# Performance work log

Hardware: AMD Instinct MI355X
Metric: run time of the kernel (lower is better)

## Reference

```python
import jax, jax.numpy as jnp
import numpy as np

T, B, M, A, H = 2048, 128, 32, 32, 64
G = M + A + H  # gate input features (mass_in_gates=True)


def _l1norm(a):
    # F.normalize(p=1, dim=-1): a / max(sum|a|, 1e-12); a is sigmoid output (>0)
    return a / jnp.maximum(jnp.sum(jnp.abs(a), axis=-1, keepdims=True), 1e-12)


def setup_inputs() -> dict:
    key = jax.random.key(0)
    ks = jax.random.split(key, 5)
    ortho = jax.nn.initializers.orthogonal()
    return {
        "x_m": jax.random.uniform(ks[0], (T, B, M), dtype=jnp.float32),
        "x_a": jax.random.normal(ks[1], (T, B, A), dtype=jnp.float32),
        "Wi": ortho(ks[2], (G, M * H), jnp.float32),  # input gate
        "bi": jnp.zeros((M * H,), jnp.float32),
        "Wr": ortho(ks[3], (G, H * H), jnp.float32),  # redistribution
        "br": jnp.zeros((H * H,), jnp.float32),
        "Wo": ortho(ks[4], (G, H), jnp.float32),      # output gate
        "bo": jnp.zeros((H,), jnp.float32),
    }


def reference(x_m, x_a, Wi, bi, Wr, br, Wo, bo):
    def step(c, xs):
        xt_m, xt_a = xs  # [B,M], [B,A]
        # NOTE: torch c.norm(1) (no dim) = scalar L1 norm of whole [B,H] tensor
        cn = c / (jnp.sum(jnp.abs(c)) + 1e-5)
        feat = jnp.concatenate([xt_m, xt_a, cn], axis=-1)  # [B,G]
        i = _l1norm(jax.nn.sigmoid(feat @ Wi + bi).reshape(-1, M, H))  # [B,M,H]
        r = _l1norm(jax.nn.sigmoid(feat @ Wr + br).reshape(-1, H, H))  # [B,H,H]
        o = jax.nn.sigmoid(feat @ Wo + bo)                              # [B,H]
        m_new = jnp.einsum('bm,bmh->bh', xt_m, i) + jnp.einsum('bk,bkh->bh', c, r)
        m_out = o * m_new
        c_new = (1.0 - o) * m_new  # subtract_outgoing_mass=True
        return c_new, (m_out, c_new)

    c0 = jnp.zeros((x_m.shape[1], H), x_m.dtype)
    _, (m_out, c) = jax.lax.scan(step, c0, (x_m, x_a))
    return m_out, c
```

## Files before the change

### kernel.cpp

```cpp
#include <hip/hip_runtime.h>
#include <hip/hip_fp16.h>


#define TT 2048
#define NBS 8
#define NUS 7
#define NWG 56

typedef _Float16 f16;
typedef _Float16 f16x8 __attribute__((ext_vector_type(8)));
typedef float f32x4 __attribute__((ext_vector_type(4)));

#define LD_RLX(p)   __hip_atomic_load((p), __ATOMIC_RELAXED, __HIP_MEMORY_SCOPE_AGENT)
#define ST_RLX(p,v) __hip_atomic_store((p), (v), __ATOMIC_RELAXED, __HIP_MEMORY_SCOPE_AGENT)

static __device__ __forceinline__ unsigned packf16(float v, unsigned tag) {
  f16 h = (f16)v;
  unsigned short s;
  __builtin_memcpy(&s, &h, 2);
  return ((unsigned)s << 16) | (tag & 0xffffu);
}
static __device__ __forceinline__ float unpackf16(unsigned u) {
  unsigned short s = (unsigned short)(u >> 16);
  f16 h;
  __builtin_memcpy(&h, &s, 2);
  return (float)h;
}
static __device__ __forceinline__ float f16bits(unsigned short s) {
  f16 h;
  __builtin_memcpy(&h, &s, 2);
  return (float)h;
}
static __device__ __forceinline__ unsigned short f16of(float v) {
  f16 h = (f16)v;
  unsigned short s;
  __builtin_memcpy(&s, &h, 2);
  return s;
}

#define OFF_WH   0u
#define SZ_WH    (97u * 8192u * 2u)
#define OFF_SLAB ((OFF_WH + SZ_WH + 255u) & ~255u)
#define SZ_SLAB  (2u * NBS * NUS * 1024u * 4u)
#define OFF_NS   (OFF_SLAB + SZ_SLAB)
#define SZ_NS    (2u * NBS * 4u)
#define ZERO_OFF OFF_SLAB
#define ZERO_LEN (SZ_SLAB + SZ_NS)

__global__ void prep_kernel(const float* __restrict__ Wi, const float* __restrict__ Wr,
                            const float* __restrict__ Wo, f16* __restrict__ Wh) {
  int idx = blockIdx.x * 256 + threadIdx.x;
  if (idx >= 97 * 8192) return;
  int g = idx & 127, h = (idx >> 7) & 63, r = idx >> 13;
  float v;
  if (r < 32)      v = Wi[g * 2048 + r * 64 + h];
  else if (r < 96) v = Wr[g * 4096 + (r - 32) * 64 + h];
  else             v = Wo[g * 64 + h];
  Wh[idx] = (f16)v;
}

__launch_bounds__(512, 1)
__global__ void mclstm_kernel(const float* __restrict__ xm, const float* __restrict__ xa,
                              const float* __restrict__ bi, const float* __restrict__ br,
                              const float* __restrict__ bo, const f16* __restrict__ Wh,
                              unsigned* __restrict__ slab, unsigned* __restrict__ nslab,
                              float* __restrict__ out) {
  const int j = blockIdx.x, tid = threadIdx.x;
  const int us = j % NUS, bs = j / NUS;
  const int w = tid >> 6, l = tid & 63, lr = l & 15, lk = l >> 4;
  const bool isO = (us == 6);

  __shared__ unsigned short craw[16][88];
  __shared__ float pslab[8][1024];
  __shared__ float nredL[8];
  __shared__ float invS;

  for (int i = tid; i < 16 * 88; i += 512) (&craw[0][0])[i] = 0;
  if (tid == 0) invS = 0.f;

  f16x8 Bf[2][4][4];
  float bu[2][4];
#pragma unroll
  for (int un = 0; un < 2; ++un) {
    int u = isO ? 96 : us * 16 + 2 * w + un;
#pragma unroll
    for (int ht = 0; ht < 4; ++ht) {
      int col = ht * 16 + lr;
      bu[un][ht] = (u < 32) ? bi[u * 64 + col]
                 : (u < 96) ? br[(u - 32) * 64 + col] : bo[col];
#pragma unroll
      for (int kk = 0; kk < 4; ++kk)
        Bf[un][ht][kk] = *(const f16x8*)(Wh + (size_t)u * 8192 + col * 128 + kk * 32 + lk * 8);
    }
  }

  const size_t xoff = (size_t)(bs * 16 + lr) * 32 + lk * 8;
  f32x4 xA0 = *(const f32x4*)(xm + xoff), xA1 = *(const f32x4*)(xm + xoff + 4);
  f32x4 xB0 = *(const f32x4*)(xa + xoff), xB1 = *(const f32x4*)(xa + xoff + 4);
  __syncthreads();

  for (int t = 0; t <= TT; ++t) {
    if (t > 0) {
      const unsigned want = (unsigned)t & 0xffffu;
      const unsigned* base = slab + ((size_t)(t & 1) * NBS + bs) * (NUS * 1024);
      const int e0 = 2 * tid;
      unsigned pv[14];
      for (;;) {
#pragma unroll
        for (int c = 0; c < 7; ++c) {
          pv[c] = LD_RLX(base + c * 1024 + e0);
          pv[7 + c] = LD_RLX(base + c * 1024 + e0 + 1);
        }
        unsigned m = 0;
#pragma unroll
        for (int c = 0; c < 14; ++c) m |= (pv[c] ^ want) & 0xffffu;
        if (m == 0) break;
        __builtin_amdgcn_s_sleep(1);
      }
      float mn0 = 0.f, mn1 = 0.f;
#pragma unroll
      for (int c = 0; c < 6; ++c) {
        mn0 += unpackf16(pv[c]);
        mn1 += unpackf16(pv[7 + c]);
      }
      const float ov0 = unpackf16(pv[6]), ov1 = unpackf16(pv[13]);
      const float cn0 = (1.0f - ov0) * mn0, cn1 = (1.0f - ov1) * mn1;
      const unsigned short h0 = f16of(cn0), h1 = f16of(cn1);
      const int b = e0 >> 6, h = e0 & 63;
      craw[b][h] = h0;
      craw[b][h + 1] = h1;
      if (isO) {
        float ns = fabsf(f16bits(h0)) + fabsf(f16bits(h1));
        ns += __shfl_xor(ns, 1, 64);
        ns += __shfl_xor(ns, 2, 64);
        ns += __shfl_xor(ns, 4, 64);
        ns += __shfl_xor(ns, 8, 64);
        ns += __shfl_xor(ns, 16, 64);
        ns += __shfl_xor(ns, 32, 64);
        if (l == 0) nredL[w] = ns;
        __syncthreads();
        if (tid == 0) {
          float nsum = 0.f;
#pragma unroll
          for (int p = 0; p < 8; ++p) nsum += nredL[p];
          ST_RLX(nslab + (t & 1) * NBS + bs, packf16(nsum, (unsigned)t));
        }
        const int bg = bs * 16 + b;
        out[(size_t)(t - 1) * 8192 + bg * 64 + h] = ov0 * mn0;
        out[(size_t)(t - 1) * 8192 + bg * 64 + h + 1] = ov1 * mn1;
        out[(size_t)(TT + t - 1) * 8192 + bg * 64 + h] = cn0;
        out[(size_t)(TT + t - 1) * 8192 + bg * 64 + h + 1] = cn1;
      }
    }
    if (t == TT) break;
    __syncthreads();

    f16x8 A0, A1, A2, A3;
#pragma unroll
    for (int i = 0; i < 4; ++i) {
      A0[i] = (f16)xA0[i]; A0[4 + i] = (f16)xA1[i];
      A1[i] = (f16)xB0[i]; A1[4 + i] = (f16)xB1[i];
    }
    {
      const unsigned short* cr = &craw[lr][0];
#pragma unroll
      for (int i = 0; i < 8; ++i) A2[i] = *(const f16*)&cr[lk * 8 + i];
#pragma unroll
      for (int i = 0; i < 8; ++i) A3[i] = *(const f16*)&cr[32 + lk * 8 + i];
    }
    if (t + 1 < TT) {
      const float* bx = xm + (size_t)(t + 1) * 4096 + xoff;
      const float* ba = xa + (size_t)(t + 1) * 4096 + xoff;
      xA0 = *(const f32x4*)bx; xA1 = *(const f32x4*)(bx + 4);
      xB0 = *(const f32x4*)ba; xB1 = *(const f32x4*)(ba + 4);
    }
    f32x4 aX[2][4], aC[2][4];
    if (!isO || w == 0) {
#pragma unroll
      for (int un = 0; un < 2; ++un)
#pragma unroll
        for (int ht = 0; ht < 4; ++ht) {
          f32x4 a = (f32x4){0.f, 0.f, 0.f, 0.f};
          a = __builtin_amdgcn_mfma_f32_16x16x32_f16(A0, Bf[un][ht][0], a, 0, 0, 0);
          a = __builtin_amdgcn_mfma_f32_16x16x32_f16(A1, Bf[un][ht][1], a, 0, 0, 0);
          aX[un][ht] = a;
          f32x4 c = (f32x4){0.f, 0.f, 0.f, 0.f};
          c = __builtin_amdgcn_mfma_f32_16x16x32_f16(A2, Bf[un][ht][2], c, 0, 0, 0);
          c = __builtin_amdgcn_mfma_f32_16x16x32_f16(A3, Bf[un][ht][3], c, 0, 0, 0);
          aC[un][ht] = c;
        }
    }

    if (t > 0 && w == 0) {
      const unsigned want = (unsigned)t & 0xffffu;
      const unsigned* nsb = nslab + (t & 1) * NBS;
      unsigned v;
      for (;;) {
        v = (l < NBS) ? LD_RLX(nsb + l) : want;
        if (__all((int)((v & 0xffffu) == want))) break;
        __builtin_amdgcn_s_sleep(1);
      }
      float ns = (l < NBS) ? unpackf16(v) : 0.f;
      ns += __shfl_xor(ns, 1, 64);
      ns += __shfl_xor(ns, 2, 64);
      ns += __shfl_xor(ns, 4, 64);
      if (l == 0) invS = __builtin_amdgcn_rcpf(ns + 1e-5f);
    }
    __syncthreads();
    const float inv = invS;

    if (!isO) {
      const float* xmtp = xm + (size_t)t * 4096;
      float contrib[4][4];
#pragma unroll
      for (int ht = 0; ht < 4; ++ht)
#pragma unroll
        for (int rr = 0; rr < 4; ++rr) contrib[ht][rr] = 0.f;
#pragma unroll
      for (int un = 0; un < 2; ++un) {
        const int u = us * 16 + 2 * w + un;
        const bool isI = (u < 32);
        const int kidx = u - 32;
#pragma unroll
        for (int rr = 0; rr < 4; ++rr) {
          const int b = lk * 4 + rr;
          float s4[4], sum = 0.f;
#pragma unroll
          for (int ht = 0; ht < 4; ++ht) {
            float z = aX[un][ht][rr] + inv * aC[un][ht][rr] + bu[un][ht];
            float sg = __builtin_amdgcn_rcpf(1.0f + __expf(-z));
            s4[ht] = sg;
            sum += sg;
          }
          float r4 = sum;
          r4 += __shfl_xor(r4, 1, 64);
          r4 += __shfl_xor(r4, 2, 64);
          r4 += __shfl_xor(r4, 4, 64);
          r4 += __shfl_xor(r4, 8, 64);
          float wr = isI ? xmtp[(size_t)(bs * 16 + b) * 32 + u] : f16bits(craw[b][kidx]);
          float sc = wr * __builtin_amdgcn_rcpf(fmaxf(r4, 1e-12f));
#pragma unroll
          for (int ht = 0; ht < 4; ++ht) contrib[ht][rr] += s4[ht] * sc;
        }
      }
#pragma unroll
      for (int ht = 0; ht < 4; ++ht)
#pragma unroll
        for (int rr = 0; rr < 4; ++rr)
          pslab[w][(lk * 4 + rr) * 64 + ht * 16 + lr] = contrib[ht][rr];
    } else if (w == 0) {
#pragma unroll
      for (int ht = 0; ht < 4; ++ht)
#pragma unroll
        for (int rr = 0; rr < 4; ++rr) {
          float z = aX[0][ht][rr] + inv * aC[0][ht][rr] + bu[0][ht];
          pslab[0][(lk * 4 + rr) * 64 + ht * 16 + lr] =
              __builtin_amdgcn_rcpf(1.0f + __expf(-z));
        }
    }
    __syncthreads();

    {
      const int e0 = 2 * tid;
      float v0, v1;
      if (!isO) {
        v0 = 0.f; v1 = 0.f;
#pragma unroll
        for (int p = 0; p < 8; ++p) {
          float2 pv2 = *(const float2*)&pslab[p][e0];
          v0 += pv2.x;
          v1 += pv2.y;
        }
      } else {
        float2 pv2 = *(const float2*)&pslab[0][e0];
        v0 = pv2.x;
        v1 = pv2.y;
      }
      const unsigned tg = (unsigned)(t + 1);
      unsigned* dst = slab + ((size_t)((t + 1) & 1) * NBS + bs) * (NUS * 1024) + us * 1024;
      ST_RLX(dst + e0, packf16(v0, tg));
      ST_RLX(dst + e0 + 1, packf16(v1, tg));
    }
    __syncthreads();
  }
}

extern "C" void kernel_launch(void* const* d_in, const int* in_sizes, int n_in,
                              void* d_out, int out_size, void* d_ws, size_t ws_size,
                              hipStream_t stream) {
  (void)in_sizes; (void)n_in; (void)out_size; (void)ws_size;
  const float* xm = (const float*)d_in[0];
  const float* xa = (const float*)d_in[1];
  const float* Wi = (const float*)d_in[2];
  const float* bi = (const float*)d_in[3];
  const float* Wr = (const float*)d_in[4];
  const float* br = (const float*)d_in[5];
  const float* Wo = (const float*)d_in[6];
  const float* bo = (const float*)d_in[7];

  char* ws = (char*)d_ws;
  f16* Wh         = (f16*)(ws + OFF_WH);
  unsigned* slab  = (unsigned*)(ws + OFF_SLAB);
  unsigned* nslab = (unsigned*)(ws + OFF_NS);

  hipMemsetAsync(ws + ZERO_OFF, 0, ZERO_LEN, stream);
  prep_kernel<<<(97 * 8192 + 255) / 256, 256, 0, stream>>>(Wi, Wr, Wo, Wh);
  mclstm_kernel<<<NWG, 512, 0, stream>>>(xm, xa, bi, br, bo, Wh, slab, nslab,
                                         (float*)d_out);
}
```

Measured before the change: 17.68 ms.

## Add per-step sentinel flags, defer output writes, prefetch input-mass scalars

Adds a small sentinel array that each workgroup sets after writing its slab partial. Consumers spin on this single flag vector, capped at SPIN_CAP iterations, before polling all 14 packed slab words, which is meant to cut polling traffic on the slab. The output-gate workgroup's global stores of m_out and c are moved off the critical path to the end of the step, after the sentinel store. Input-gate workgroups also prefetch their x_m scalars at the top of the step rather than loading them inside the sigmoid loop. The trade-off is an extra barrier-adjacent atomic store per step, plus an extra load round-trip before the existing slab poll.

```diff
diff --git a/kernel.cpp b/kernel.cpp
--- a/kernel.cpp
+++ b/kernel.cpp
@@ -6,6 +6,7 @@
 #define NBS 8
 #define NUS 7
 #define NWG 56
+#define SPIN_CAP (1 << 16)
 
 typedef _Float16 f16;
 typedef _Float16 f16x8 __attribute__((ext_vector_type(8)));
@@ -44,8 +45,10 @@
 #define SZ_SLAB  (2u * NBS * NUS * 1024u * 4u)
 #define OFF_NS   (OFF_SLAB + SZ_SLAB)
 #define SZ_NS    (2u * NBS * 4u)
+#define OFF_SENT (OFF_NS + SZ_NS)
+#define SZ_SENT  (2u * NBS * 32u * 4u)
 #define ZERO_OFF OFF_SLAB
-#define ZERO_LEN (SZ_SLAB + SZ_NS)
+#define ZERO_LEN (SZ_SLAB + SZ_NS + SZ_SENT)
 
 __global__ void prep_kernel(const float* __restrict__ Wi, const float* __restrict__ Wr,
                             const float* __restrict__ Wo, f16* __restrict__ Wh) {
@@ -64,11 +67,12 @@
                               const float* __restrict__ bi, const float* __restrict__ br,
                               const float* __restrict__ bo, const f16* __restrict__ Wh,
                               unsigned* __restrict__ slab, unsigned* __restrict__ nslab,
-                              float* __restrict__ out) {
+                              unsigned* __restrict__ sent, float* __restrict__ out) {
   const int j = blockIdx.x, tid = threadIdx.x;
   const int us = j % NUS, bs = j / NUS;
   const int w = tid >> 6, l = tid & 63, lr = l & 15, lk = l >> 4;
   const bool isO = (us == 6);
+  const bool isIWG = (us < 2);
 
   __shared__ unsigned short craw[16][88];
   __shared__ float pslab[8][1024];
@@ -99,9 +103,30 @@
   f32x4 xB0 = *(const f32x4*)(xa + xoff), xB1 = *(const f32x4*)(xa + xoff + 4);
   __syncthreads();
 
+  float ov0 = 0.f, ov1 = 0.f, mn0 = 0.f, mn1 = 0.f, cn0 = 0.f, cn1 = 0.f;
+
   for (int t = 0; t <= TT; ++t) {
+    float xw[2][4];
+    if (isIWG && t < TT) {
+      const float* xmtp = xm + (size_t)t * 4096;
+#pragma unroll
+      for (int rr = 0; rr < 4; ++rr) {
+        const size_t ro = (size_t)(bs * 16 + lk * 4 + rr) * 32 + us * 16 + 2 * w;
+        xw[0][rr] = xmtp[ro];
+        xw[1][rr] = xmtp[ro + 1];
+      }
+    }
+
     if (t > 0) {
       const unsigned want = (unsigned)t & 0xffffu;
+      {
+        const unsigned* sb = sent + ((size_t)(t & 1) * NBS + bs) * 32;
+        for (int it = 0; it < SPIN_CAP; ++it) {
+          unsigned v = (l < NUS) ? LD_RLX(sb + l) : want;
+          if (__all((int)((v & 0xffffu) == want))) break;
+          __builtin_amdgcn_s_sleep(1);
+        }
+      }
       const unsigned* base = slab + ((size_t)(t & 1) * NBS + bs) * (NUS * 1024);
       const int e0 = 2 * tid;
       unsigned pv[14];
@@ -117,14 +142,16 @@
         if (m == 0) break;
         __builtin_amdgcn_s_sleep(1);
       }
-      float mn0 = 0.f, mn1 = 0.f;
+      mn0 = 0.f; mn1 = 0.f;
 #pragma unroll
       for (int c = 0; c < 6; ++c) {
         mn0 += unpackf16(pv[c]);
         mn1 += unpackf16(pv[7 + c]);
       }
-      const float ov0 = unpackf16(pv[6]), ov1 = unpackf16(pv[13]);
-      const float cn0 = (1.0f - ov0) * mn0, cn1 = (1.0f - ov1) * mn1;
+      ov0 = unpackf16(pv[6]);
+      ov1 = unpackf16(pv[13]);
+      cn0 = (1.0f - ov0) * mn0;
+      cn1 = (1.0f - ov1) * mn1;
       const unsigned short h0 = f16of(cn0), h1 = f16of(cn1);
       const int b = e0 >> 6, h = e0 & 63;
       craw[b][h] = h0;
@@ -145,14 +172,19 @@
           for (int p = 0; p < 8; ++p) nsum += nredL[p];
           ST_RLX(nslab + (t & 1) * NBS + bs, packf16(nsum, (unsigned)t));
         }
+      }
+    }
+    if (t == TT) {
+      if (isO) {
+        const int e0 = 2 * tid, b = e0 >> 6, h = e0 & 63;
         const int bg = bs * 16 + b;
         out[(size_t)(t - 1) * 8192 + bg * 64 + h] = ov0 * mn0;
         out[(size_t)(t - 1) * 8192 + bg * 64 + h + 1] = ov1 * mn1;
         out[(size_t)(TT + t - 1) * 8192 + bg * 64 + h] = cn0;
         out[(size_t)(TT + t - 1) * 8192 + bg * 64 + h + 1] = cn1;
       }
-    }
-    if (t == TT) break;
+      break;
+    }
     __syncthreads();
 
     f16x8 A0, A1, A2, A3;
@@ -210,7 +242,6 @@
     const float inv = invS;
 
     if (!isO) {
-      const float* xmtp = xm + (size_t)t * 4096;
       float contrib[4][4];
 #pragma unroll
       for (int ht = 0; ht < 4; ++ht)
@@ -218,9 +249,7 @@
         for (int rr = 0; rr < 4; ++rr) contrib[ht][rr] = 0.f;
 #pragma unroll
       for (int un = 0; un < 2; ++un) {
-        const int u = us * 16 + 2 * w + un;
-        const bool isI = (u < 32);
-        const int kidx = u - 32;
+        const int kidx = us * 16 + 2 * w + un - 32;
 #pragma unroll
         for (int rr = 0; rr < 4; ++rr) {
           const int b = lk * 4 + rr;
@@ -237,7 +266,7 @@
           r4 += __shfl_xor(r4, 2, 64);
           r4 += __shfl_xor(r4, 4, 64);
           r4 += __shfl_xor(r4, 8, 64);
-          float wr = isI ? xmtp[(size_t)(bs * 16 + b) * 32 + u] : f16bits(craw[b][kidx]);
+          float wr = isIWG ? xw[un][rr] : f16bits(craw[b][kidx]);
           float sc = wr * __builtin_amdgcn_rcpf(fmaxf(r4, 1e-12f));
 #pragma unroll
           for (int ht = 0; ht < 4; ++ht) contrib[ht][rr] += s4[ht] * sc;
@@ -282,6 +311,17 @@
       ST_RLX(dst + e0 + 1, packf16(v1, tg));
     }
     __syncthreads();
+    if (tid == 0)
+      ST_RLX(sent + ((size_t)((t + 1) & 1) * NBS + bs) * 32 + us, (unsigned)(t + 1));
+
+    if (isO && t > 0) {
+      const int e0 = 2 * tid, b = e0 >> 6, h = e0 & 63;
+      const int bg = bs * 16 + b;
+      out[(size_t)(t - 1) * 8192 + bg * 64 + h] = ov0 * mn0;
+      out[(size_t)(t - 1) * 8192 + bg * 64 + h + 1] = ov1 * mn1;
+      out[(size_t)(TT + t - 1) * 8192 + bg * 64 + h] = cn0;
+      out[(size_t)(TT + t - 1) * 8192 + bg * 64 + h + 1] = cn1;
+    }
   }
 }
 
@@ -302,9 +342,10 @@
   f16* Wh         = (f16*)(ws + OFF_WH);
   unsigned* slab  = (unsigned*)(ws + OFF_SLAB);
   unsigned* nslab = (unsigned*)(ws + OFF_NS);
+  unsigned* sent  = (unsigned*)(ws + OFF_SENT);
 
   hipMemsetAsync(ws + ZERO_OFF, 0, ZERO_LEN, stream);
   prep_kernel<<<(97 * 8192 + 255) / 256, 256, 0, stream>>>(Wi, Wr, Wo, Wh);
-  mclstm_kernel<<<NWG, 512, 0, stream>>>(xm, xa, bi, br, bo, Wh, slab, nslab,
+  mclstm_kernel<<<NWG, 512, 0, stream>>>(xm, xa, bi, br, bo, Wh, slab, nslab, sent,
                                          (float*)d_out);
 }
```

After: 28.27 ms. 1.6x slower.

## Hoist input-side MFMAs before slab wait and add sentinel-based polling

Applied to the files above, without the earlier changes.

Moves the x-dependent MFMA products and the next-step x loads ahead of the inter-workgroup slab wait, so they overlap the wait for the previous step's recurrent state. It prefetches the per-unit xm weights into registers, adds a light per-wave sentinel poll before the full slab read, and drops the trailing barrier of the loop. It also changes the launch attributes to amdgpu_waves_per_eu(2,2), which relaxes the register budget. The risks are higher register pressure from keeping aX live across the wait, and a possible shared-memory race from removing the end-of-loop barrier.

```diff
diff --git a/kernel.cpp b/kernel.cpp
--- a/kernel.cpp
+++ b/kernel.cpp
@@ -59,7 +59,8 @@
   Wh[idx] = (f16)v;
 }
 
-__launch_bounds__(512, 1)
+__launch_bounds__(512)
+__attribute__((amdgpu_waves_per_eu(2, 2)))
 __global__ void mclstm_kernel(const float* __restrict__ xm, const float* __restrict__ xa,
                               const float* __restrict__ bi, const float* __restrict__ br,
                               const float* __restrict__ bo, const f16* __restrict__ Wh,
@@ -69,6 +70,7 @@
   const int us = j % NUS, bs = j / NUS;
   const int w = tid >> 6, l = tid & 63, lr = l & 15, lk = l >> 4;
   const bool isO = (us == 6);
+  const bool isIWG = (us < 2);
 
   __shared__ unsigned short craw[16][88];
   __shared__ float pslab[8][1024];
@@ -100,9 +102,54 @@
   __syncthreads();
 
   for (int t = 0; t <= TT; ++t) {
+    float xw[2][4];
+    f32x4 aX[2][4];
+    if (t < TT) {
+      if (isIWG) {
+        const float* xmtp = xm + (size_t)t * 4096;
+#pragma unroll
+        for (int rr = 0; rr < 4; ++rr) {
+          const size_t ro = (size_t)(bs * 16 + lk * 4 + rr) * 32 + us * 16 + 2 * w;
+          xw[0][rr] = xmtp[ro];
+          xw[1][rr] = xmtp[ro + 1];
+        }
+      }
+      f16x8 A0, A1;
+#pragma unroll
+      for (int i = 0; i < 4; ++i) {
+        A0[i] = (f16)xA0[i]; A0[4 + i] = (f16)xA1[i];
+        A1[i] = (f16)xB0[i]; A1[4 + i] = (f16)xB1[i];
+      }
+      if (t + 1 < TT) {
+        const float* bx = xm + (size_t)(t + 1) * 4096 + xoff;
+        const float* ba = xa + (size_t)(t + 1) * 4096 + xoff;
+        xA0 = *(const f32x4*)bx; xA1 = *(const f32x4*)(bx + 4);
+        xB0 = *(const f32x4*)ba; xB1 = *(const f32x4*)(ba + 4);
+      }
+      if (!isO || w == 0) {
+#pragma unroll
+        for (int un = 0; un < 2; ++un)
+#pragma unroll
+          for (int ht = 0; ht < 4; ++ht) {
+            f32x4 a = (f32x4){0.f, 0.f, 0.f, 0.f};
+            a = __builtin_amdgcn_mfma_f32_16x16x32_f16(A0, Bf[un][ht][0], a, 0, 0, 0);
+            a = __builtin_amdgcn_mfma_f32_16x16x32_f16(A1, Bf[un][ht][1], a, 0, 0, 0);
+            aX[un][ht] = a;
+          }
+      }
+    }
+
     if (t > 0) {
       const unsigned want = (unsigned)t & 0xffffu;
       const unsigned* base = slab + ((size_t)(t & 1) * NBS + bs) * (NUS * 1024);
+      {
+        const unsigned* gp = base + l * 1024 + 128 * w;
+        for (;;) {
+          unsigned v = (l < NUS) ? LD_RLX(gp) : want;
+          if (__all((int)((v & 0xffffu) == want))) break;
+          __builtin_amdgcn_s_sleep(1);
+        }
+      }
       const int e0 = 2 * tid;
       unsigned pv[14];
       for (;;) {
@@ -155,12 +202,7 @@
     if (t == TT) break;
     __syncthreads();
 
-    f16x8 A0, A1, A2, A3;
-#pragma unroll
-    for (int i = 0; i < 4; ++i) {
-      A0[i] = (f16)xA0[i]; A0[4 + i] = (f16)xA1[i];
-      A1[i] = (f16)xB0[i]; A1[4 + i] = (f16)xB1[i];
-    }
+    f16x8 A2, A3;
     {
       const unsigned short* cr = &craw[lr][0];
 #pragma unroll
@@ -168,22 +210,12 @@
 #pragma unroll
       for (int i = 0; i < 8; ++i) A3[i] = *(const f16*)&cr[32 + lk * 8 + i];
     }
-    if (t + 1 < TT) {
-      const float* bx = xm + (size_t)(t + 1) * 4096 + xoff;
-      const float* ba = xa + (size_t)(t + 1) * 4096 + xoff;
-      xA0 = *(const f32x4*)bx; xA1 = *(const f32x4*)(bx + 4);
-      xB0 = *(const f32x4*)ba; xB1 = *(const f32x4*)(ba + 4);
-    }
-    f32x4 aX[2][4], aC[2][4];
+    f32x4 aC[2][4];
     if (!isO || w == 0) {
 #pragma unroll
       for (int un = 0; un < 2; ++un)
 #pragma unroll
         for (int ht = 0; ht < 4; ++ht) {
-          f32x4 a = (f32x4){0.f, 0.f, 0.f, 0.f};
-          a = __builtin_amdgcn_mfma_f32_16x16x32_f16(A0, Bf[un][ht][0], a, 0, 0, 0);
-          a = __builtin_amdgcn_mfma_f32_16x16x32_f16(A1, Bf[un][ht][1], a, 0, 0, 0);
-          aX[un][ht] = a;
           f32x4 c = (f32x4){0.f, 0.f, 0.f, 0.f};
           c = __builtin_amdgcn_mfma_f32_16x16x32_f16(A2, Bf[un][ht][2], c, 0, 0, 0);
           c = __builtin_amdgcn_mfma_f32_16x16x32_f16(A3, Bf[un][ht][3], c, 0, 0, 0);
@@ -210,7 +242,6 @@
     const float inv = invS;
 
     if (!isO) {
-      const float* xmtp = xm + (size_t)t * 4096;
       float contrib[4][4];
 #pragma unroll
       for (int ht = 0; ht < 4; ++ht)
@@ -218,9 +249,7 @@
         for (int rr = 0; rr < 4; ++rr) contrib[ht][rr] = 0.f;
 #pragma unroll
       for (int un = 0; un < 2; ++un) {
-        const int u = us * 16 + 2 * w + un;
-        const bool isI = (u < 32);
-        const int kidx = u - 32;
+        const int kidx = us * 16 + 2 * w + un - 32;
 #pragma unroll
         for (int rr = 0; rr < 4; ++rr) {
           const int b = lk * 4 + rr;
@@ -237,7 +266,7 @@
           r4 += __shfl_xor(r4, 2, 64);
           r4 += __shfl_xor(r4, 4, 64);
           r4 += __shfl_xor(r4, 8, 64);
-          float wr = isI ? xmtp[(size_t)(bs * 16 + b) * 32 + u] : f16bits(craw[b][kidx]);
+          float wr = isIWG ? xw[un][rr] : f16bits(craw[b][kidx]);
           float sc = wr * __builtin_amdgcn_rcpf(fmaxf(r4, 1e-12f));
 #pragma unroll
           for (int ht = 0; ht < 4; ++ht) contrib[ht][rr] += s4[ht] * sc;
@@ -281,7 +310,6 @@
       ST_RLX(dst + e0, packf16(v0, tg));
       ST_RLX(dst + e0 + 1, packf16(v1, tg));
     }
-    __syncthreads();
   }
 }
 
```

Result: no change. 17.72 ms (+0.2%).

## Pin persistent workgroups to one XCC and poll flags with sc0 loads

Applied to the files above, without the earlier changes.

Launches a large grid and lets workgroups on XCC 0 claim the 56 worker slots through an atomic counter, so every cooperating workgroup sits on one chiplet and shares its L2. Workgroups on other XCCs wait until the slots are taken and then exit. Flag polling and publishing now use inline-asm global loads and stores with sc0 and fall back to agent-scope relaxed accesses, so cross-workgroup signalling can stay in the shared cache instead of the slower device-coherent path. The cost is launching and retiring many extra workgroups, and correctness depends on XCC 0 supplying 56 resident workgroups; if it does not, the fallback path may place workers on other XCCs while readers still try the sc0 path first.

```diff
diff --git a/kernel.cpp b/kernel.cpp
--- a/kernel.cpp
+++ b/kernel.cpp
@@ -6,6 +6,7 @@
 #define NBS 8
 #define NUS 7
 #define NWG 56
+#define GRID 2048
 
 typedef _Float16 f16;
 typedef _Float16 f16x8 __attribute__((ext_vector_type(8)));
@@ -38,14 +39,56 @@
   return s;
 }
 
-#define OFF_WH   0u
-#define SZ_WH    (97u * 8192u * 2u)
-#define OFF_SLAB ((OFF_WH + SZ_WH + 255u) & ~255u)
-#define SZ_SLAB  (2u * NBS * NUS * 1024u * 4u)
-#define OFF_NS   (OFF_SLAB + SZ_SLAB)
-#define SZ_NS    (2u * NBS * 4u)
-#define ZERO_OFF OFF_SLAB
-#define ZERO_LEN (SZ_SLAB + SZ_NS)
+static __device__ __forceinline__ unsigned ld_sc0(const unsigned* p) {
+  unsigned v;
+  asm volatile("global_load_dword %0, %1, off sc0\n\ts_waitcnt vmcnt(0)"
+               : "=v"(v) : "v"(p) : "memory");
+  return v;
+}
+static __device__ __forceinline__ void st_sc0(unsigned* p, unsigned v) {
+  asm volatile("global_store_dword %0, %1, off sc0" :: "v"(p), "v"(v) : "memory");
+}
+static __device__ __forceinline__ void sweep14_sc0(const unsigned* base, int e0,
+                                                   unsigned pv[14]) {
+  const unsigned* p0 = base + e0;
+  const unsigned* p1 = base + 1024 + e0;
+  const unsigned* p2 = base + 2048 + e0;
+  const unsigned* p3 = base + 3072 + e0;
+  const unsigned* p4 = base + 4096 + e0;
+  const unsigned* p5 = base + 5120 + e0;
+  const unsigned* p6 = base + 6144 + e0;
+  asm volatile(
+      "global_load_dword %0, %14, off sc0\n\t"
+      "global_load_dword %7, %14, off offset:4 sc0\n\t"
+      "global_load_dword %1, %15, off sc0\n\t"
+      "global_load_dword %8, %15, off offset:4 sc0\n\t"
+      "global_load_dword %2, %16, off sc0\n\t"
+      "global_load_dword %9, %16, off offset:4 sc0\n\t"
+      "global_load_dword %3, %17, off sc0\n\t"
+      "global_load_dword %10, %17, off offset:4 sc0\n\t"
+      "global_load_dword %4, %18, off sc0\n\t"
+      "global_load_dword %11, %18, off offset:4 sc0\n\t"
+      "global_load_dword %5, %19, off sc0\n\t"
+      "global_load_dword %12, %19, off offset:4 sc0\n\t"
+      "global_load_dword %6, %20, off sc0\n\t"
+      "global_load_dword %13, %20, off offset:4 sc0\n\t"
+      "s_waitcnt vmcnt(0)"
+      : "=&v"(pv[0]), "=&v"(pv[1]), "=&v"(pv[2]), "=&v"(pv[3]), "=&v"(pv[4]),
+        "=&v"(pv[5]), "=&v"(pv[6]), "=&v"(pv[7]), "=&v"(pv[8]), "=&v"(pv[9]),
+        "=&v"(pv[10]), "=&v"(pv[11]), "=&v"(pv[12]), "=&v"(pv[13])
+      : "v"(p0), "v"(p1), "v"(p2), "v"(p3), "v"(p4), "v"(p5), "v"(p6)
+      : "memory");
+}
+
+#define OFF_WH    0u
+#define SZ_WH     (97u * 8192u * 2u)
+#define OFF_SLAB  ((OFF_WH + SZ_WH + 255u) & ~255u)
+#define SZ_SLAB   (2u * NBS * NUS * 1024u * 4u)
+#define OFF_NS    (OFF_SLAB + SZ_SLAB)
+#define SZ_NS     (2u * NBS * 4u)
+#define OFF_CLAIM ((OFF_NS + SZ_NS + 255u) & ~255u)
+#define ZERO_OFF  OFF_SLAB
+#define ZERO_LEN  (OFF_CLAIM - OFF_SLAB + 256u)
 
 __global__ void prep_kernel(const float* __restrict__ Wi, const float* __restrict__ Wr,
                             const float* __restrict__ Wo, f16* __restrict__ Wh) {
@@ -64,9 +107,33 @@
                               const float* __restrict__ bi, const float* __restrict__ br,
                               const float* __restrict__ bo, const f16* __restrict__ Wh,
                               unsigned* __restrict__ slab, unsigned* __restrict__ nslab,
-                              float* __restrict__ out) {
-  const int j = blockIdx.x, tid = threadIdx.x;
-  const int us = j % NUS, bs = j / NUS;
+                              unsigned* __restrict__ claim, float* __restrict__ out) {
+  const int tid = threadIdx.x;
+  __shared__ int slotS;
+
+  if (tid == 0) {
+    unsigned xcc;
+    asm("s_getreg_b32 %0, hwreg(HW_REG_XCC_ID)" : "=s"(xcc));
+    int s = -1;
+    if (xcc == 0) {
+      s = (int)__hip_atomic_fetch_add(claim, 1u, __ATOMIC_RELAXED,
+                                      __HIP_MEMORY_SCOPE_AGENT);
+    } else {
+      for (int it = 0; it < (1 << 14); ++it) {
+        if (LD_RLX(claim) >= (unsigned)NWG) break;
+        __builtin_amdgcn_s_sleep(4);
+      }
+      if (LD_RLX(claim) < (unsigned)NWG)
+        s = (int)__hip_atomic_fetch_add(claim, 1u, __ATOMIC_RELAXED,
+                                        __HIP_MEMORY_SCOPE_AGENT);
+    }
+    slotS = s;
+  }
+  __syncthreads();
+  const int slot = slotS;
+  if (slot < 0 || slot >= NWG) return;
+
+  const int us = slot % NUS, bs = slot / NUS;
   const int w = tid >> 6, l = tid & 63, lr = l & 15, lk = l >> 4;
   const bool isO = (us == 6);
 
@@ -106,12 +173,17 @@
       const int e0 = 2 * tid;
       unsigned pv[14];
       for (;;) {
+        sweep14_sc0(base, e0, pv);
+        unsigned m = 0;
+#pragma unroll
+        for (int c = 0; c < 14; ++c) m |= (pv[c] ^ want) & 0xffffu;
+        if (m == 0) break;
 #pragma unroll
         for (int c = 0; c < 7; ++c) {
           pv[c] = LD_RLX(base + c * 1024 + e0);
           pv[7 + c] = LD_RLX(base + c * 1024 + e0 + 1);
         }
-        unsigned m = 0;
+        m = 0;
 #pragma unroll
         for (int c = 0; c < 14; ++c) m |= (pv[c] ^ want) & 0xffffu;
         if (m == 0) break;
@@ -143,7 +215,10 @@
           float nsum = 0.f;
 #pragma unroll
           for (int p = 0; p < 8; ++p) nsum += nredL[p];
-          ST_RLX(nslab + (t & 1) * NBS + bs, packf16(nsum, (unsigned)t));
+          unsigned nv = packf16(nsum, (unsigned)t);
+          unsigned* np = nslab + (t & 1) * NBS + bs;
+          st_sc0(np, nv);
+          ST_RLX(np, nv);
         }
         const int bg = bs * 16 + b;
         out[(size_t)(t - 1) * 8192 + bg * 64 + h] = ov0 * mn0;
@@ -194,9 +269,11 @@
     if (t > 0 && w == 0) {
       const unsigned want = (unsigned)t & 0xffffu;
       const unsigned* nsb = nslab + (t & 1) * NBS;
-      unsigned v;
+      unsigned v = want;
       for (;;) {
-        v = (l < NBS) ? LD_RLX(nsb + l) : want;
+        if (l < NBS) v = ld_sc0(nsb + l);
+        if (__all((int)((v & 0xffffu) == want))) break;
+        if (l < NBS) v = LD_RLX(nsb + l);
         if (__all((int)((v & 0xffffu) == want))) break;
         __builtin_amdgcn_s_sleep(1);
       }
@@ -278,8 +355,11 @@
       }
       const unsigned tg = (unsigned)(t + 1);
       unsigned* dst = slab + ((size_t)((t + 1) & 1) * NBS + bs) * (NUS * 1024) + us * 1024;
-      ST_RLX(dst + e0, packf16(v0, tg));
-      ST_RLX(dst + e0 + 1, packf16(v1, tg));
+      const unsigned q0 = packf16(v0, tg), q1 = packf16(v1, tg);
+      st_sc0(dst + e0, q0);
+      st_sc0(dst + e0 + 1, q1);
+      ST_RLX(dst + e0, q0);
+      ST_RLX(dst + e0 + 1, q1);
     }
     __syncthreads();
   }
@@ -302,9 +382,10 @@
   f16* Wh         = (f16*)(ws + OFF_WH);
   unsigned* slab  = (unsigned*)(ws + OFF_SLAB);
   unsigned* nslab = (unsigned*)(ws + OFF_NS);
+  unsigned* claim = (unsigned*)(ws + OFF_CLAIM);
 
   hipMemsetAsync(ws + ZERO_OFF, 0, ZERO_LEN, stream);
   prep_kernel<<<(97 * 8192 + 255) / 256, 256, 0, stream>>>(Wi, Wr, Wo, Wh);
-  mclstm_kernel<<<NWG, 512, 0, stream>>>(xm, xa, bi, br, bo, Wh, slab, nslab,
-                                         (float*)d_out);
-}
+  mclstm_kernel<<<GRID, 512, 0, stream>>>(xm, xa, bi, br, bo, Wh, slab, nslab,
+                                          claim, (float*)d_out);
+}
```

Result: slower. 23.59 ms (+33.4%).
